# Kernel optimization log

Measured on AMD Instinct MI355X. Metric: run time of the kernel, lower is better.

## Reference

```python
import jax, jax.numpy as jnp
import numpy as np

N_MOLS = 2048
ATOMS_PER_MOL = 32
BONDS_PER_MOL = 32  # undirected
N_ATOMS = N_MOLS * ATOMS_PER_MOL            # 65536
N_BONDS = 2 * N_MOLS * BONDS_PER_MOL        # 131072 directed
ATOM_FDIM = 133
BOND_RAW_FDIM = 14
BOND_FDIM = ATOM_FDIM + BOND_RAW_FDIM       # 147 (chemprop: f_atoms[src] ++ bond feats)
HIDDEN = 512
DEPTH = 3
CLS_HID = 512


def setup_inputs() -> dict:
    key = jax.random.key(0)
    ks = jax.random.split(key, 12)
    rng = np.random.default_rng(0)

    # --- graph structure: per-molecule random undirected bonds, both directions ---
    offs = (np.arange(N_MOLS) * ATOMS_PER_MOL)[:, None]
    u = (rng.integers(0, ATOMS_PER_MOL, (N_MOLS, BONDS_PER_MOL)) + offs).ravel()
    v = (rng.integers(0, ATOMS_PER_MOL, (N_MOLS, BONDS_PER_MOL)) + offs).ravel()
    bond_src = np.stack([u, v], axis=1).ravel().astype(np.int32)  # bond 2e: u->v, 2e+1: v->u
    bond_dst = np.stack([v, u], axis=1).ravel().astype(np.int32)
    b2revb = (np.arange(N_BONDS) ^ 1).astype(np.int32)
    atom_mol_id = np.repeat(np.arange(N_MOLS), ATOMS_PER_MOL).astype(np.int32)

    f_atoms = jax.random.normal(ks[0], (N_ATOMS, ATOM_FDIM), jnp.float32)
    bond_feat = jax.random.normal(ks[1], (N_BONDS, BOND_RAW_FDIM), jnp.float32)
    f_bonds = jnp.concatenate([f_atoms[jnp.asarray(bond_src)], bond_feat], axis=1)  # [B, 147]

    def lin(k, fan_in, fan_out):
        return jax.random.normal(k, (fan_in, fan_out), jnp.float32) / np.sqrt(fan_in)

    return {
        "f_atoms": f_atoms,
        "f_bonds": f_bonds,
        "W_i": lin(ks[2], BOND_FDIM, HIDDEN),
        "W_h": lin(ks[3], HIDDEN, HIDDEN),
        "W_o": lin(ks[4], ATOM_FDIM + HIDDEN, HIDDEN),
        "c1_W": lin(ks[5], HIDDEN, CLS_HID), "c1_b": jnp.zeros((CLS_HID,), jnp.float32),
        "c2_W": lin(ks[6], CLS_HID, CLS_HID), "c2_b": jnp.zeros((CLS_HID,), jnp.float32),
        "c3_W": lin(ks[7], CLS_HID, CLS_HID), "c3_b": jnp.zeros((CLS_HID,), jnp.float32),
        "out_W": lin(ks[8], CLS_HID, 1), "out_b": jnp.zeros((1,), jnp.float32),
        "bond_src": jnp.asarray(bond_src),
        "bond_dst": jnp.asarray(bond_dst),
        "b2revb": jnp.asarray(b2revb),
        "atom_mol_id": jnp.asarray(atom_mol_id),
    }


def reference(f_atoms, f_bonds, W_i, W_h, W_o,
              c1_W, c1_b, c2_W, c2_b, c3_W, c3_b, out_W, out_b,
              bond_src, bond_dst, b2revb, atom_mol_id):
    relu = jax.nn.relu
    seg = jax.ops.segment_sum

    inp = f_bonds @ W_i                      # [B, H]
    msg = relu(inp)
    for _ in range(DEPTH - 1):
        # sum of incoming bond messages at each atom (bond u->v is incoming to v)
        a_msg = seg(msg, bond_dst, num_segments=N_ATOMS)   # [A, H]
        msg = a_msg[bond_src] - msg[b2revb]                # exclude reverse bond
        msg = relu(inp + msg @ W_h)

    a_msg = seg(msg, bond_dst, num_segments=N_ATOMS)
    atom_h = relu(jnp.concatenate([f_atoms, a_msg], axis=1) @ W_o)  # [A, H]

    # mean aggregation per molecule
    mol_sum = seg(atom_h, atom_mol_id, num_segments=N_MOLS)
    counts = seg(jnp.ones((N_ATOMS,), atom_h.dtype), atom_mol_id, num_segments=N_MOLS)
    mol_vec = mol_sum / counts[:, None]      # [M, H]

    h = relu(mol_vec @ c1_W + c1_b)
    h = relu(h @ c2_W + c2_b)
    h = relu(h @ c3_W + c3_b)
    h = relu(h)  # extra ReLU in original Sequential (no-op after ReLU, kept for fidelity)
    logits = h @ out_W + out_b               # [M, 1]
    return logits
```

## Files before the change

### kernel.cpp

```cpp
#include <hip/hip_runtime.h>
#include <stdint.h>

typedef unsigned short u16;
typedef __attribute__((ext_vector_type(8))) short short8;
typedef __attribute__((ext_vector_type(4))) float f32x4;

static __device__ __forceinline__ float b2f(u16 u) {
    union { unsigned int i; float f; } x; x.i = ((unsigned int)u) << 16; return x.f;
}
static __device__ __forceinline__ u16 f2b(float f) {
    unsigned int x = __builtin_bit_cast(unsigned int, f);
    x += 0x7fffu + ((x >> 16) & 1u);
    return (u16)(x >> 16);
}
static __device__ __forceinline__ unsigned int cvt_pk(float lo, float hi) {
    unsigned int r;
    asm("v_cvt_pk_bf16_f32 %0, %1, %2" : "=v"(r) : "v"(lo), "v"(hi));
    return r;
}
static __device__ __forceinline__ void async16(const u16* g, u16* l) {
    __builtin_amdgcn_global_load_lds(
        (const __attribute__((address_space(1))) unsigned int*)g,
        (__attribute__((address_space(3))) unsigned int*)l, 16, 0, 0);
}

__global__ __launch_bounds__(512, 1) void gemm_ip_k(
    const u16* __restrict__ Abonds,
    const u16* __restrict__ Wc,
    const u16* __restrict__ amsg,
    u16* __restrict__ msg,
    const int* __restrict__ bsrc)
{
    __shared__ u16 lA[2][128 * 64];
    __shared__ u16 lBp[8][2][64 * 64];
    const int t = threadIdx.x;
    const int r0 = blockIdx.x * 128;

    const int arow = t >> 3;
    const int al = (t & 7) ^ (arow & 7);
    const u16* agA = Abonds + (size_t)(r0 + arow) * 192 + al * 8;
    const int e0 = r0 + arow, e1 = r0 + 64 + arow;
    const u16* ar0 = amsg + (size_t)bsrc[e0] * 512 + al * 8;
    const u16* ar1 = amsg + (size_t)bsrc[e1] * 512 + al * 8;
    const u16* mr0 = msg + (size_t)(e0 ^ 1) * 512 + al * 8;
    const u16* mr1 = msg + (size_t)(e1 ^ 1) * 512 + al * 8;

    const int wid = t >> 6, lane = t & 63;
    const int wcol = wid * 64;
    const int lrow = lane & 15, lk = lane >> 4;
    u16* myB = &lBp[wid][0][0];
    const int bl = (lane & 7) ^ ((lane >> 3) & 7);
    const u16* bgWp = Wc + (size_t)(wcol + (lane >> 3)) * 704 + bl * 8;

    f32x4 acc[8][4] = {};
    short8 av0, av1, mv0, mv1;

#define STAGE_B(k0, buf) { _Pragma("unroll") for (int i = 0; i < 8; ++i) \
        async16(bgWp + (size_t)(i * 8) * 704 + (k0), myB + (buf) * 4096 + (i * 64 + lane) * 8); }
#define STAGE_A1(k0, buf) { \
        async16(agA + (k0), &lA[buf][t * 8]); \
        async16(agA + (size_t)64 * 192 + (k0), &lA[buf][(512 + t) * 8]); }
#define LOAD_A2(k0) { av0 = *(const short8*)(ar0 + ((k0) - 192)); \
                      mv0 = *(const short8*)(mr0 + ((k0) - 192)); \
                      av1 = *(const short8*)(ar1 + ((k0) - 192)); \
                      mv1 = *(const short8*)(mr1 + ((k0) - 192)); }
#define WRITE_A2(buf) { union { short8 s; unsigned int u[4]; } o; \
        _Pragma("unroll") for (int p = 0; p < 4; ++p) \
            o.u[p] = cvt_pk(b2f((u16)av0[2*p]) - b2f((u16)mv0[2*p]), \
                            b2f((u16)av0[2*p+1]) - b2f((u16)mv0[2*p+1])); \
        *(short8*)&lA[buf][t * 8] = o.s; \
        _Pragma("unroll") for (int p = 0; p < 4; ++p) \
            o.u[p] = cvt_pk(b2f((u16)av1[2*p]) - b2f((u16)mv1[2*p]), \
                            b2f((u16)av1[2*p+1]) - b2f((u16)mv1[2*p+1])); \
        *(short8*)&lA[buf][(512 + t) * 8] = o.s; }
#define CMP_H(buf, kk) { short8 af[8], bf[4]; \
        _Pragma("unroll") for (int m = 0; m < 8; ++m) { \
            int row = m * 16 + lrow; \
            int sl = ((kk) >> 3) + lk; \
            af[m] = *(const short8*)&lA[buf][row * 64 + ((sl ^ (row & 7)) * 8)]; } \
        _Pragma("unroll") for (int n = 0; n < 4; ++n) { \
            int row = n * 16 + lrow; \
            int sl = ((kk) >> 3) + lk; \
            bf[n] = *(const short8*)(myB + (buf) * 4096 + row * 64 + ((sl ^ (row & 7)) * 8)); } \
        _Pragma("unroll") for (int m = 0; m < 8; ++m) \
        _Pragma("unroll") for (int n = 0; n < 4; ++n) \
            acc[m][n] = __builtin_amdgcn_mfma_f32_16x16x32_bf16(af[m], bf[n], acc[m][n], 0, 0, 0); }

    STAGE_B(0, 0)
    STAGE_A1(0, 0)

#pragma unroll
    for (int s = 0; s < 11; ++s) {
        const int cur = s & 1;
        const int k1 = (s + 1) * 64;
        if (s < 10) {
            if (k1 < 192) {
                STAGE_B(k1, cur ^ 1)
                STAGE_A1(k1, cur ^ 1)
                asm volatile("s_waitcnt vmcnt(10)" ::: "memory");
            } else {
                LOAD_A2(k1)
                STAGE_B(k1, cur ^ 1)
                asm volatile("s_waitcnt vmcnt(12)" ::: "memory");
            }
        } else {
            asm volatile("s_waitcnt vmcnt(0)" ::: "memory");
        }
        __builtin_amdgcn_s_barrier();
        __builtin_amdgcn_s_setprio(1);
        CMP_H(cur, 0)
        if (s < 10 && k1 >= 192) WRITE_A2(cur ^ 1)
        CMP_H(cur, 32)
        __builtin_amdgcn_s_setprio(0);
        if (s < 10) {
            asm volatile("s_waitcnt lgkmcnt(0)" ::: "memory");
            if (s == 0) __builtin_amdgcn_s_barrier();
        }
    }
#undef STAGE_B
#undef STAGE_A1
#undef LOAD_A2
#undef WRITE_A2
#undef CMP_H

    const int rr0 = r0 + (lane >> 4) * 4;
    const int cc0 = wcol + (lane & 15);
#pragma unroll
    for (int m = 0; m < 8; ++m)
#pragma unroll
        for (int n = 0; n < 4; ++n)
#pragma unroll
            for (int r = 0; r < 4; ++r)
                msg[(size_t)(rr0 + m * 16 + r) * 512 + cc0 + n * 16] =
                    f2b(fmaxf(acc[m][n][r], 0.f));
}

template<int MODE>
__global__ __launch_bounds__(512, 1) void gemm_p_k(
    const u16* __restrict__ A1, const u16* __restrict__ Bt,
    const u16* __restrict__ A2, u16* __restrict__ Cout, u16* __restrict__ mOut)
{
    constexpr int NST = (MODE == 0) ? 3 : 11;
    __shared__ u16 lA[2][128 * 64];
    __shared__ u16 lBp[8][2][64 * 64];
    const int t = threadIdx.x;
    const int r0 = blockIdx.x * 128;

    const int arow = t >> 3;
    const int al = (t & 7) ^ (arow & 7);
    const size_t row0 = (size_t)(r0 + arow), row1 = row0 + 64;

    const int wid = t >> 6, lane = t & 63;
    const int wcol = wid * 64;
    const int lrow = lane & 15, lk = lane >> 4;
    u16* myB = &lBp[wid][0][0];
    const int bl = (lane & 7) ^ ((lane >> 3) & 7);
    const u16* bgWp = Bt + (size_t)(wcol + (lane >> 3)) * 704 + bl * 8;

    f32x4 acc[8][4] = {};
    short8 a0r, a1r;

#define STAGE_B(k0, buf) { _Pragma("unroll") for (int i = 0; i < 8; ++i) \
        async16(bgWp + (size_t)(i * 8) * 704 + (k0), myB + (buf) * 4096 + (i * 64 + lane) * 8); }
#define ASRC(k0, rw) ((MODE == 0) ? (A1 + (rw) * 192 + (k0) + al * 8) \
        : (((k0) + al * 8 < 160) ? (A1 + (rw) * 160 + (k0) + al * 8) \
        : (A2 + (rw) * 512 + (((k0) + al * 8 - 160 < 504) ? ((k0) + al * 8 - 160) : 504))))
#define STAGE_A0(k0, buf) { async16(ASRC(k0, row0), &lA[buf][t * 8]); \
                            async16(ASRC(k0, row1), &lA[buf][(512 + t) * 8]); }
#define LOAD_A(k0) { a0r = *(const short8*)ASRC(k0, row0); \
                     a1r = *(const short8*)ASRC(k0, row1); }
#define WRITE_A(buf) { *(short8*)&lA[buf][t * 8] = a0r; \
                       *(short8*)&lA[buf][(512 + t) * 8] = a1r; }
#define CMP_H(buf, kk) { short8 af[8], bf[4]; \
        _Pragma("unroll") for (int m = 0; m < 8; ++m) { \
            int row = m * 16 + lrow; \
            int sl = ((kk) >> 3) + lk; \
            af[m] = *(const short8*)&lA[buf][row * 64 + ((sl ^ (row & 7)) * 8)]; } \
        _Pragma("unroll") for (int n = 0; n < 4; ++n) { \
            int row = n * 16 + lrow; \
            int sl = ((kk) >> 3) + lk; \
            bf[n] = *(const short8*)(myB + (buf) * 4096 + row * 64 + ((sl ^ (row & 7)) * 8)); } \
        _Pragma("unroll") for (int m = 0; m < 8; ++m) \
        _Pragma("unroll") for (int n = 0; n < 4; ++n) \
            acc[m][n] = __builtin_amdgcn_mfma_f32_16x16x32_bf16(af[m], bf[n], acc[m][n], 0, 0, 0); }

    STAGE_B(0, 0)
    STAGE_A0(0, 0)

#pragma unroll
    for (int s = 0; s < NST; ++s) {
        const int cur = s & 1;
        const int k1 = (s + 1) * 64;
        if (s < NST - 1) {
            LOAD_A(k1)
            STAGE_B(k1, cur ^ 1)
            asm volatile("s_waitcnt vmcnt(10)" ::: "memory");
        } else {
            asm volatile("s_waitcnt vmcnt(0)" ::: "memory");
        }
        __builtin_amdgcn_s_barrier();
        __builtin_amdgcn_s_setprio(1);
        CMP_H(cur, 0)
        if (s < NST - 1) WRITE_A(cur ^ 1)
        CMP_H(cur, 32)
        __builtin_amdgcn_s_setprio(0);
        if (s < NST - 1) {
            asm volatile("s_waitcnt lgkmcnt(0)" ::: "memory");
        }
    }
#undef STAGE_B
#undef ASRC
#undef STAGE_A0
#undef LOAD_A
#undef WRITE_A
#undef CMP_H

    if constexpr (MODE == 0) {
        const int rr0 = r0 + (lane >> 4) * 4;
        const int cc0 = wcol + (lane & 15);
#pragma unroll
        for (int m = 0; m < 8; ++m)
#pragma unroll
            for (int n = 0; n < 4; ++n)
#pragma unroll
                for (int r = 0; r < 4; ++r)
                    Cout[(size_t)(rr0 + m * 16 + r) * 512 + cc0 + n * 16] =
                        f2b(fmaxf(acc[m][n][r], 0.f));
    } else {
        const int molBase = r0 >> 5;
#pragma unroll
        for (int n = 0; n < 4; ++n) {
            const int col = wcol + n * 16 + (lane & 15);
#pragma unroll
            for (int j = 0; j < 4; ++j) {
                float s = 0.f;
#pragma unroll
                for (int r = 0; r < 4; ++r)
                    s += fmaxf(acc[2 * j][n][r], 0.f) + fmaxf(acc[2 * j + 1][n][r], 0.f);
                s += __shfl_xor(s, 16);
                s += __shfl_xor(s, 32);
                if ((lane >> 4) == 0)
                    mOut[(size_t)(molBase + j) * 512 + col] = f2b(s * 0.03125f);
            }
        }
    }
}

__global__ __launch_bounds__(256, 2) void gemm_oop_k(
    const u16* __restrict__ A, const u16* __restrict__ Bt, u16* __restrict__ C,
    int M, int N, int K, int lda, int ldb, int nbn)
{
    __shared__ u16 lA[128 * 64];
    __shared__ u16 lB[128 * 64];
    const int tid = threadIdx.x;
    const int gid = blockIdx.x;
    const int q = (int)gridDim.x >> 3;
    const int gbi = (gid & 7) * q + (gid >> 3);
    const int mb = gbi / nbn, nb = gbi % nbn;

    const int wid = tid >> 6, lane = tid & 63;
    const int wr = (wid >> 1) * 64, wc = (wid & 1) * 64;
    const int lrow = lane & 15, lko = (lane >> 4) * 8;

    f32x4 acc[4][4] = {};
    const int srow = tid >> 3;
    const int scol = (tid & 7) * 8;
    const u16* ag = A + (size_t)(mb * 128 + srow) * lda + scol;
    const u16* bg = Bt + (size_t)(nb * 128 + srow) * ldb + scol;
    u16* la = &lA[tid * 8];
    u16* lb = &lB[tid * 8];

    for (int k0 = 0; k0 < K; k0 += 64) {
#pragma unroll
        for (int i = 0; i < 4; ++i) {
            async16(ag + (size_t)(i * 32) * lda + k0, la + i * 2048);
            async16(bg + (size_t)(i * 32) * ldb + k0, lb + i * 2048);
        }
        __syncthreads();
#pragma unroll
        for (int kk = 0; kk < 64; kk += 32) {
            short8 af[4], bf[4];
#pragma unroll
            for (int m = 0; m < 4; ++m)
                af[m] = *(const short8*)&lA[(wr + m * 16 + lrow) * 64 + kk + lko];
#pragma unroll
            for (int n = 0; n < 4; ++n)
                bf[n] = *(const short8*)&lB[(wc + n * 16 + lrow) * 64 + kk + lko];
#pragma unroll
            for (int m = 0; m < 4; ++m)
#pragma unroll
                for (int n = 0; n < 4; ++n)
                    acc[m][n] = __builtin_amdgcn_mfma_f32_16x16x32_bf16(af[m], bf[n], acc[m][n], 0, 0, 0);
        }
        __syncthreads();
    }

    const int r0 = mb * 128 + wr + (lane >> 4) * 4;
    const int c0 = nb * 128 + wc + (lane & 15);
#pragma unroll
    for (int m = 0; m < 4; ++m)
#pragma unroll
        for (int n = 0; n < 4; ++n)
#pragma unroll
            for (int r = 0; r < 4; ++r)
                C[(size_t)(r0 + m * 16 + r) * N + c0 + n * 16] = f2b(fmaxf(acc[m][n][r], 0.f));
}

__global__ __launch_bounds__(256) void segsum_k(
    const u16* __restrict__ msg, const int* __restrict__ bdst, u16* __restrict__ out)
{
    __shared__ float acc[32][512];
    const int m = blockIdx.x, t = threadIdx.x;
    const int c = t * 2;
#pragma unroll
    for (int a = 0; a < 32; ++a) { acc[a][c] = 0.f; acc[a][c + 1] = 0.f; }
    const int eb = m * 64;
#pragma unroll 4
    for (int ee = 0; ee < 64; ++ee) {
        int d = bdst[eb + ee] & 31;
        unsigned int v = *(const unsigned int*)&msg[(size_t)(eb + ee) * 512 + c];
        acc[d][c]     += b2f((u16)(v & 0xffffu));
        acc[d][c + 1] += b2f((u16)(v >> 16));
    }
#pragma unroll
    for (int a = 0; a < 32; ++a)
        *(unsigned int*)&out[(size_t)(m * 32 + a) * 512 + c] = cvt_pk(acc[a][c], acc[a][c + 1]);
}

__global__ void cast_bonds_k(const float* __restrict__ fb, u16* __restrict__ Ab) {
    const int total = 131072 * 24;
    for (int g = blockIdx.x * blockDim.x + threadIdx.x; g < total; g += gridDim.x * blockDim.x) {
        int b = g / 24, s = g - b * 24;
        const float* src = fb + (size_t)b * 147 + s * 8;
        short8 o;
#pragma unroll
        for (int j = 0; j < 8; ++j) {
            int cc = s * 8 + j;
            o[j] = (short)f2b(cc < 147 ? src[j] : 0.f);
        }
        *(short8*)&Ab[(size_t)g * 8] = o;
    }
}

__global__ void cast_atoms_k(const float* __restrict__ fa, u16* __restrict__ Af) {
    const int total = 65536 * 20;
    for (int g = blockIdx.x * blockDim.x + threadIdx.x; g < total; g += gridDim.x * blockDim.x) {
        int a = g / 20, s = g - a * 20;
        const float* src = fa + (size_t)a * 133 + s * 8;
        short8 o;
#pragma unroll
        for (int j = 0; j < 8; ++j) {
            int cc = s * 8 + j;
            o[j] = (short)f2b(cc < 133 ? src[j] : 0.f);
        }
        *(short8*)&Af[(size_t)a * 160 + s * 8] = o;
    }
}

__global__ void prep_w_k(const float* __restrict__ Wi, const float* __restrict__ Wh,
                         const float* __restrict__ Wo, const float* __restrict__ c1,
                         const float* __restrict__ c2, const float* __restrict__ c3,
                         u16* __restrict__ Wcomb, u16* __restrict__ WoT,
                         u16* __restrict__ c1T, u16* __restrict__ c2T, u16* __restrict__ c3T)
{
    const int total = 360448 * 2 + 262144 * 3;
    for (int idx = blockIdx.x * blockDim.x + threadIdx.x; idx < total; idx += gridDim.x * blockDim.x) {
        if (idx < 360448) {
            int n = idx / 704, k = idx % 704;
            float v = 0.f;
            if (k < 147) v = Wi[(size_t)k * 512 + n];
            else if (k >= 192) v = Wh[(size_t)(k - 192) * 512 + n];
            Wcomb[idx] = f2b(v);
        } else if (idx < 720896) {
            int j = idx - 360448;
            int n = j / 704, k = j % 704;
            float v = 0.f;
            if (k < 133) v = Wo[(size_t)k * 512 + n];
            else if (k >= 160 && k < 672) v = Wo[(size_t)(k - 27) * 512 + n];
            WoT[j] = f2b(v);
        } else {
            int j = idx - 720896;
            int which = j / 262144, jj = j % 262144;
            int n = jj / 512, k = jj % 512;
            const float* W = (which == 0) ? c1 : (which == 1) ? c2 : c3;
            u16* Wt = (which == 0) ? c1T : (which == 1) ? c2T : c3T;
            Wt[jj] = f2b(W[(size_t)k * 512 + n]);
        }
    }
}

__global__ void logits_k(const u16* __restrict__ h, const float* __restrict__ ow,
                         const float* __restrict__ ob, float* __restrict__ out) {
    const int row = blockIdx.x * 4 + (threadIdx.x >> 6);
    const int lane = threadIdx.x & 63;
    const u16* hr = h + (size_t)row * 512 + lane * 8;
    float s = 0.f;
#pragma unroll
    for (int j = 0; j < 8; ++j) s += b2f(hr[j]) * ow[lane * 8 + j];
#pragma unroll
    for (int o = 32; o > 0; o >>= 1) s += __shfl_down(s, o);
    if (lane == 0) out[row] = s + ob[0];
}

extern "C" void kernel_launch(void* const* d_in, const int* in_sizes, int n_in,
                              void* d_out, int out_size, void* d_ws, size_t ws_size,
                              hipStream_t stream) {
    const float* f_atoms = (const float*)d_in[0];
    const float* f_bonds = (const float*)d_in[1];
    const float* W_i  = (const float*)d_in[2];
    const float* W_h  = (const float*)d_in[3];
    const float* W_o  = (const float*)d_in[4];
    const float* c1W  = (const float*)d_in[5];
    const float* c2W  = (const float*)d_in[7];
    const float* c3W  = (const float*)d_in[9];
    const float* outW = (const float*)d_in[11];
    const float* outB = (const float*)d_in[12];
    const int* bsrc = (const int*)d_in[13];
    const int* bdst = (const int*)d_in[14];
    float* out = (float*)d_out;
    (void)in_sizes; (void)n_in; (void)out_size;

    if (ws_size < 254672896u) return;

    char* w = (char*)d_ws;
    size_t off = 0;
    auto alloc = [&](size_t bytes) {
        size_t o = (off + 255) & ~(size_t)255; off = o + bytes; return (void*)(w + o);
    };

    u16* msg    = (u16*)alloc(134217728);
    u16* amsg   = (u16*)alloc(67108864);
    u16* Abonds = (u16*)alloc(50331648);
    u16* Wcomb  = (u16*)alloc(720896);
    u16* WoT    = (u16*)alloc(720896);
    u16* c1T    = (u16*)alloc(524288);
    u16* c2T    = (u16*)alloc(524288);
    u16* c3T    = (u16*)alloc(524288);
    u16* Afeat = Abonds;
    u16* molv  = msg;
    u16* h1    = molv + 1048576;
    u16* h2    = h1 + 1048576;
    u16* h3    = h2 + 1048576;

    prep_w_k<<<1024, 256, 0, stream>>>(W_i, W_h, W_o, c1W, c2W, c3W, Wcomb, WoT, c1T, c2T, c3T);
    cast_bonds_k<<<4096, 256, 0, stream>>>(f_bonds, Abonds);

    gemm_p_k<0><<<1024, 512, 0, stream>>>(Abonds, Wcomb, nullptr, msg, nullptr);

    for (int it = 0; it < 2; ++it) {
        segsum_k<<<2048, 256, 0, stream>>>(msg, bdst, amsg);
        gemm_ip_k<<<1024, 512, 0, stream>>>(Abonds, Wcomb, amsg, msg, bsrc);
    }

    segsum_k<<<2048, 256, 0, stream>>>(msg, bdst, amsg);
    cast_atoms_k<<<2048, 256, 0, stream>>>(f_atoms, Afeat);
    gemm_p_k<2><<<512, 512, 0, stream>>>(Afeat, WoT, amsg, nullptr, molv);

    gemm_oop_k<<<64, 256, 0, stream>>>(molv, c1T, h1, 2048, 512, 512, 512, 512, 4);
    gemm_oop_k<<<64, 256, 0, stream>>>(h1, c2T, h2, 2048, 512, 512, 512, 512, 4);
    gemm_oop_k<<<64, 256, 0, stream>>>(h2, c3T, h3, 2048, 512, 512, 512, 512, 4);
    logits_k<<<512, 256, 0, stream>>>(h3, outW, outB, out);
}
```

Before: 532.8 us.

## Fuse per-atom segment sums into GEMM epilogues using sorted bond permutation

Removes the standalone segsum kernels and computes each atom's incoming-message sum inside the bond GEMM epilogues. Each wave stages its ReLU output tile in LDS, then walks the bonds in destination-sorted order, emitting run-length sums to amsg and zeroing atoms that receive no bonds. A small sort_prep kernel builds the per-molecule permutation, and the last message-passing GEMM skips writing msg because only the aggregated sums are consumed. This cuts the repeated global read and write of the full message tensor, in exchange for a serial, shuffle-heavy epilogue and a kernel that reads and writes amsg in the same launch (safe only because bonds never cross molecule blocks).

```diff
diff --git a/kernel.cpp b/kernel.cpp
--- a/kernel.cpp
+++ b/kernel.cpp
@@ -24,12 +24,42 @@
         (__attribute__((address_space(3))) unsigned int*)l, 16, 0, 0);
 }
 
+#define SEGSUM_EPI(MOLBASE, amsgOut) { \
+    asm volatile("s_waitcnt lgkmcnt(0)" ::: "memory"); \
+    _Pragma("unroll") for (int m_ = 0; m_ < 8; ++m_) \
+    _Pragma("unroll") for (int n_ = 0; n_ < 4; ++n_) \
+    _Pragma("unroll") for (int r_ = 0; r_ < 4; ++r_) { \
+        int row = m_ * 16 + (lane >> 4) * 4 + r_; \
+        int c_ = n_ * 16 + (lane & 15); \
+        myB[row * 64 + (c_ ^ (((row >> 2) & 3) << 4))] = f2b(fmaxf(acc[m_][n_][r_], 0.f)); } \
+    asm volatile("s_waitcnt lgkmcnt(0)" ::: "memory"); \
+    int pe0_ = perm[(MOLBASE) * 64 + lane]; \
+    int d0_ = bdst[(MOLBASE) * 64 + pe0_] & 31; \
+    int pe1_ = perm[(MOLBASE) * 64 + 64 + lane]; \
+    int d1_ = bdst[(MOLBASE) * 64 + 64 + pe1_] & 31; \
+    _Pragma("unroll") for (int g_ = 0; g_ < 2; ++g_) { \
+        float run_ = 0.f; unsigned int cov_ = 0; \
+        _Pragma("unroll") for (int ss = 0; ss < 64; ++ss) { \
+            int pe_ = __shfl(g_ ? pe1_ : pe0_, ss); \
+            int d_  = __shfl(g_ ? d1_ : d0_, ss); \
+            int row = g_ * 64 + pe_; \
+            run_ += b2f(myB[row * 64 + (lane ^ (((row >> 2) & 3) << 4))]); \
+            int dn_ = (ss < 63) ? __shfl(g_ ? d1_ : d0_, ss + 1) : -1; \
+            if (d_ != dn_) { \
+                amsgOut[((size_t)((MOLBASE) + g_) * 32 + d_) * 512 + wcol + lane] = f2b(run_); \
+                run_ = 0.f; cov_ |= 1u << d_; } } \
+        _Pragma("unroll") for (int a_ = 0; a_ < 32; ++a_) \
+            if (!((cov_ >> a_) & 1)) \
+                amsgOut[((size_t)((MOLBASE) + g_) * 32 + a_) * 512 + wcol + lane] = 0; } }
+
+template<bool WRITEC>
 __global__ __launch_bounds__(512, 1) void gemm_ip_k(
     const u16* __restrict__ Abonds,
     const u16* __restrict__ Wc,
-    const u16* __restrict__ amsg,
+    u16* __restrict__ amsg,
     u16* __restrict__ msg,
-    const int* __restrict__ bsrc)
+    const int* __restrict__ bsrc, const int* __restrict__ bdst,
+    const unsigned char* __restrict__ perm)
 {
     __shared__ u16 lA[2][128 * 64];
     __shared__ u16 lBp[8][2][64 * 64];
@@ -123,22 +153,26 @@
 #undef WRITE_A2
 #undef CMP_H
 
-    const int rr0 = r0 + (lane >> 4) * 4;
-    const int cc0 = wcol + (lane & 15);
-#pragma unroll
-    for (int m = 0; m < 8; ++m)
-#pragma unroll
-        for (int n = 0; n < 4; ++n)
-#pragma unroll
-            for (int r = 0; r < 4; ++r)
-                msg[(size_t)(rr0 + m * 16 + r) * 512 + cc0 + n * 16] =
-                    f2b(fmaxf(acc[m][n][r], 0.f));
+    if constexpr (WRITEC) {
+        const int rr0 = r0 + (lane >> 4) * 4;
+        const int cc0 = wcol + (lane & 15);
+#pragma unroll
+        for (int m = 0; m < 8; ++m)
+#pragma unroll
+            for (int n = 0; n < 4; ++n)
+#pragma unroll
+                for (int r = 0; r < 4; ++r)
+                    msg[(size_t)(rr0 + m * 16 + r) * 512 + cc0 + n * 16] =
+                        f2b(fmaxf(acc[m][n][r], 0.f));
+    }
+    SEGSUM_EPI(blockIdx.x * 2, amsg)
 }
 
 template<int MODE>
 __global__ __launch_bounds__(512, 1) void gemm_p_k(
     const u16* __restrict__ A1, const u16* __restrict__ Bt,
-    const u16* __restrict__ A2, u16* __restrict__ Cout, u16* __restrict__ mOut)
+    const u16* __restrict__ A2, u16* __restrict__ Cout, u16* __restrict__ mOut,
+    const int* __restrict__ bdst, const unsigned char* __restrict__ perm)
 {
     constexpr int NST = (MODE == 0) ? 3 : 11;
     __shared__ u16 lA[2][128 * 64];
@@ -226,6 +260,7 @@
                 for (int r = 0; r < 4; ++r)
                     Cout[(size_t)(rr0 + m * 16 + r) * 512 + cc0 + n * 16] =
                         f2b(fmaxf(acc[m][n][r], 0.f));
+        SEGSUM_EPI(blockIdx.x * 2, mOut)
     } else {
         const int molBase = r0 >> 5;
 #pragma unroll
@@ -306,25 +341,21 @@
                 C[(size_t)(r0 + m * 16 + r) * N + c0 + n * 16] = f2b(fmaxf(acc[m][n][r], 0.f));
 }
 
-__global__ __launch_bounds__(256) void segsum_k(
-    const u16* __restrict__ msg, const int* __restrict__ bdst, u16* __restrict__ out)
-{
-    __shared__ float acc[32][512];
-    const int m = blockIdx.x, t = threadIdx.x;
-    const int c = t * 2;
-#pragma unroll
-    for (int a = 0; a < 32; ++a) { acc[a][c] = 0.f; acc[a][c + 1] = 0.f; }
-    const int eb = m * 64;
-#pragma unroll 4
-    for (int ee = 0; ee < 64; ++ee) {
-        int d = bdst[eb + ee] & 31;
-        unsigned int v = *(const unsigned int*)&msg[(size_t)(eb + ee) * 512 + c];
-        acc[d][c]     += b2f((u16)(v & 0xffffu));
-        acc[d][c + 1] += b2f((u16)(v >> 16));
-    }
-#pragma unroll
-    for (int a = 0; a < 32; ++a)
-        *(unsigned int*)&out[(size_t)(m * 32 + a) * 512 + c] = cvt_pk(acc[a][c], acc[a][c + 1]);
+__global__ void sort_prep_k(const int* __restrict__ bdst, unsigned char* __restrict__ perm) {
+    int m = blockIdx.x * blockDim.x + threadIdx.x;
+    if (m >= 2048) return;
+    int eb = m * 64;
+    int cnt[32];
+#pragma unroll
+    for (int a = 0; a < 32; ++a) cnt[a] = 0;
+    for (int e = 0; e < 64; ++e) cnt[bdst[eb + e] & 31]++;
+    int pos[32]; int run = 0;
+#pragma unroll
+    for (int a = 0; a < 32; ++a) { pos[a] = run; run += cnt[a]; }
+    for (int e = 0; e < 64; ++e) {
+        int d = bdst[eb + e] & 31;
+        perm[eb + pos[d]++] = (unsigned char)e;
+    }
 }
 
 __global__ void cast_bonds_k(const float* __restrict__ fb, u16* __restrict__ Ab) {
@@ -420,7 +451,7 @@
     float* out = (float*)d_out;
     (void)in_sizes; (void)n_in; (void)out_size;
 
-    if (ws_size < 254672896u) return;
+    if (ws_size < 254810112u) return;
 
     char* w = (char*)d_ws;
     size_t off = 0;
@@ -436,6 +467,7 @@
     u16* c1T    = (u16*)alloc(524288);
     u16* c2T    = (u16*)alloc(524288);
     u16* c3T    = (u16*)alloc(524288);
+    unsigned char* perm = (unsigned char*)alloc(131072);
     u16* Afeat = Abonds;
     u16* molv  = msg;
     u16* h1    = molv + 1048576;
@@ -444,17 +476,15 @@
 
     prep_w_k<<<1024, 256, 0, stream>>>(W_i, W_h, W_o, c1W, c2W, c3W, Wcomb, WoT, c1T, c2T, c3T);
     cast_bonds_k<<<4096, 256, 0, stream>>>(f_bonds, Abonds);
-
-    gemm_p_k<0><<<1024, 512, 0, stream>>>(Abonds, Wcomb, nullptr, msg, nullptr);
-
-    for (int it = 0; it < 2; ++it) {
-        segsum_k<<<2048, 256, 0, stream>>>(msg, bdst, amsg);
-        gemm_ip_k<<<1024, 512, 0, stream>>>(Abonds, Wcomb, amsg, msg, bsrc);
-    }
-
-    segsum_k<<<2048, 256, 0, stream>>>(msg, bdst, amsg);
+    sort_prep_k<<<8, 256, 0, stream>>>(bdst, perm);
+
+    gemm_p_k<0><<<1024, 512, 0, stream>>>(Abonds, Wcomb, nullptr, msg, amsg, bdst, perm);
+
+    gemm_ip_k<true><<<1024, 512, 0, stream>>>(Abonds, Wcomb, amsg, msg, bsrc, bdst, perm);
+    gemm_ip_k<false><<<1024, 512, 0, stream>>>(Abonds, Wcomb, amsg, msg, bsrc, bdst, perm);
+
     cast_atoms_k<<<2048, 256, 0, stream>>>(f_atoms, Afeat);
-    gemm_p_k<2><<<512, 512, 0, stream>>>(Afeat, WoT, amsg, nullptr, molv);
+    gemm_p_k<2><<<512, 512, 0, stream>>>(Afeat, WoT, amsg, nullptr, molv, bdst, perm);
 
     gemm_oop_k<<<64, 256, 0, stream>>>(molv, c1T, h1, 2048, 512, 512, 512, 512, 4);
     gemm_oop_k<<<64, 256, 0, stream>>>(h1, c2T, h2, 2048, 512, 512, 512, 512, 4);
```

After: 642.5 us. +20.6%, slower.
